# Performance work log

Measured on AMD Instinct MI355X. Metric: run time of the kernel, lower is better.

Reference implementation:

```python
import jax, jax.numpy as jnp
import numpy as np

H = 512


def setup_inputs() -> dict:
    key = jax.random.key(0)
    ks = jax.random.split(key, 20)
    B, S, T, V, WD = 128, 80, 28, 8000, 1024
    sc = 0.02
    return {
        "encoder_hidden_state": jax.random.normal(ks[0], (1, B, H), jnp.float32),
        "encoder_outputs": jax.random.normal(ks[1], (B, S, H), jnp.float32),
        "target_sentences": jax.random.randint(ks[2], (B, T), 0, V),
        "training_steps": -200,
        "emb": jax.random.normal(ks[3], (V, WD), jnp.float32) * sc,
        "fc1_w": jax.random.normal(ks[4], (H, 2 * H), jnp.float32) * sc,
        "fc1_b": jnp.zeros((H,), jnp.float32),
        "fc2_w": jax.random.normal(ks[5], (H, H), jnp.float32) * sc,
        "fc2_b": jnp.zeros((H,), jnp.float32),
        "fc3_w": jax.random.normal(ks[6], (H, H), jnp.float32) * sc,
        "fc3_b": jnp.zeros((H,), jnp.float32),
        "fc4_w": jax.random.normal(ks[7], (H, H), jnp.float32) * sc,
        "fc4_b": jnp.zeros((H,), jnp.float32),
        "attn_w": jax.random.normal(ks[8], (H,), jnp.float32) * sc,
        "w_ih": jax.random.normal(ks[9], (4 * H, H + WD), jnp.float32) * sc,
        "w_hh": jax.random.normal(ks[10], (4 * H, H), jnp.float32) * sc,
        "b_ih": jnp.zeros((4 * H,), jnp.float32),
        "b_hh": jnp.zeros((4 * H,), jnp.float32),
        "out_w": jax.random.normal(ks[11], (V, H), jnp.float32) * sc,
        "out_b": jnp.zeros((V,), jnp.float32),
    }


def reference(encoder_hidden_state, encoder_outputs, target_sentences, training_steps,
              emb, fc1_w, fc1_b, fc2_w, fc2_b, fc3_w, fc3_b, fc4_w, fc4_b,
              attn_w, w_ih, w_hh, b_ih, b_hh, out_w, out_b):
    # With training_steps=-200, teacher-forcing threshold expit(-9.15)~1e-4, so
    # random.uniform(0.05,0.995) > threshold always holds -> target embedding used every step.
    tgt_emb = emb[target_sentences]              # (B, T, WD)
    xs = jnp.swapaxes(tgt_emb[:, :-1], 0, 1)     # (T-1, B, WD)
    h0 = encoder_hidden_state[0]                 # (B, H)
    c0 = jnp.zeros_like(h0)

    def step(carry, x_t):
        h, c = carry
        # additive-style attention: 4 stacked Linear layers (no nonlinearity, as in source)
        hs = jnp.broadcast_to(h[:, None, :], encoder_outputs.shape)
        z = jnp.concatenate([encoder_outputs, hs], axis=-1)      # (B, S, 2H)
        a = z @ fc1_w.T + fc1_b
        a = a @ fc2_w.T + fc2_b
        a = a @ fc3_w.T + fc3_b
        a = a @ fc4_w.T + fc4_b
        scores = a @ attn_w                                       # (B, S)
        wts = jax.nn.softmax(scores, axis=1)
        ctx = jnp.einsum('bs,bsd->bd', wts, encoder_outputs)      # (B, H)
        # single LSTM step (torch gate order i, f, g, o)
        li = jnp.concatenate([x_t, ctx], axis=1)                  # (B, WD+H)
        gates = li @ w_ih.T + b_ih + h @ w_hh.T + b_hh
        i_, f_, g_, o_ = jnp.split(gates, 4, axis=1)
        c_new = jax.nn.sigmoid(f_) * c + jax.nn.sigmoid(i_) * jnp.tanh(g_)
        h_new = jax.nn.sigmoid(o_) * jnp.tanh(c_new)
        logits = h_new @ out_w.T + out_b                          # (B, V)
        return (h_new, c_new), logits

    _, logits = jax.lax.scan(step, (h0, c0), xs)                  # (T-1, B, V)
    logits = jnp.swapaxes(logits, 0, 1)                           # (B, T-1, V)
    preds = jnp.argmax(logits, axis=2)
    return logits, preds
```

## Files before the change

### kernel.cpp

```cpp
#include <hip/hip_runtime.h>
#include <math.h>

#define BB 128
#define SS 80
#define HH 512
#define TT 27
#define TFULL 28
#define VV 8000

typedef __attribute__((ext_vector_type(4))) float f32x4;
typedef __attribute__((ext_vector_type(8))) short bfrag;

#define OFF_VA   0
#define OFF_VB   512
#define OFF_U    1024
#define OFF_PART 1536
#define OFF_CTX  17920
#define OFF_GB   83456
#define OFF_XG   345600
#define OFF_BAR  7423488
#define FP32_WS_FLOATS 7489536
#define O_H3     0
#define O_WHI    3670016
#define O_WLO    4718592
#define O_R      5767168
#define O_A3X    O_R
#define O_B3X    (O_R + 10616832)
#define O_B3L    O_R

__device__ __forceinline__ unsigned short f2bf(float x) {
    unsigned int u = __float_as_uint(x);
    unsigned int r = (u + 0x7fff + ((u >> 16) & 1)) >> 16;
    return (unsigned short)r;
}
__device__ __forceinline__ float bf2f(unsigned short h) {
    return __uint_as_float(((unsigned int)h) << 16);
}
__device__ __forceinline__ void gload16(void* lds, const void* g) {
    __builtin_amdgcn_global_load_lds(
        (__attribute__((address_space(1))) void*)g,
        (__attribute__((address_space(3))) void*)lds, 16, 0, 0);
}
__device__ __forceinline__ void gload16s(void* lds, const void* g) {
    __builtin_amdgcn_global_load_lds(
        (__attribute__((address_space(1))) void*)g,
        (__attribute__((address_space(3))) void*)lds, 16, 0, 1);
}

__global__ __launch_bounds__(256) void zero_bar(unsigned* b) {
    int i = blockIdx.x * 256 + threadIdx.x;
    if (i < 16512) b[i] = 0u;
}

__global__ __launch_bounds__(256) void conv_split(
    const float* __restrict__ src, int ld, int koff, int K,
    int mode, int bside, const int* __restrict__ gidx,
    unsigned short* __restrict__ dst)
{
    int r = blockIdx.x;
    int sr = r;
    if (mode == 1) { int b = r & 127, t = r >> 7; sr = gidx[b * TFULL + t]; }
    const float* s = src + (size_t)sr * ld + koff;
    unsigned short* d = dst + (size_t)r * (3 * K);
    int off_mid = bside ? 2 * K : K;
    int off_lo  = bside ? K : 2 * K;
    for (int c = threadIdx.x * 4; c < K; c += 1024) {
        float4 v = *(const float4*)(s + c);
        ushort4 hi, lo;
        hi.x = f2bf(v.x); lo.x = f2bf(v.x - bf2f(hi.x));
        hi.y = f2bf(v.y); lo.y = f2bf(v.y - bf2f(hi.y));
        hi.z = f2bf(v.z); lo.z = f2bf(v.z - bf2f(hi.z));
        hi.w = f2bf(v.w); lo.w = f2bf(v.w - bf2f(hi.w));
        *(ushort4*)(d + c) = hi;
        *(ushort4*)(d + off_mid + c) = hi;
        *(ushort4*)(d + off_lo + c) = lo;
    }
}

__global__ __launch_bounds__(256) void conv_splitc(
    const float* __restrict__ src, unsigned short* __restrict__ dst)
{
    int r = blockIdx.x;
    const float* s = src + (size_t)r * 512;
    unsigned short* d = dst + (size_t)r * 1024;
    int c = threadIdx.x * 2;
    float2 v = *(const float2*)(s + c);
    unsigned short hx = f2bf(v.x), hy = f2bf(v.y);
    d[c] = hx; d[c + 1] = hy;
    d[512 + c] = f2bf(v.x - bf2f(hx));
    d[512 + c + 1] = f2bf(v.y - bf2f(hy));
}

__global__ __launch_bounds__(256) void conv_splitw(
    const float* __restrict__ src,
    unsigned short* __restrict__ whi, unsigned short* __restrict__ wlo)
{
    int r = blockIdx.x;
    int sr = (r & 3) * 512 + (r >> 2);
    const float* s = src + (size_t)sr * 512;
    int c = threadIdx.x * 2;
    float2 v = *(const float2*)(s + c);
    unsigned short hx = f2bf(v.x), hy = f2bf(v.y);
    whi[(size_t)r * 512 + c] = hx;
    whi[(size_t)r * 512 + c + 1] = hy;
    wlo[(size_t)r * 512 + c] = f2bf(v.x - bf2f(hx));
    wlo[(size_t)r * 512 + c + 1] = f2bf(v.y - bf2f(hy));
}

__global__ __launch_bounds__(256) void gemm_bf16_nt(
    int M, int N, int K3,
    const unsigned short* __restrict__ A3, int astride, int ahalf,
    const unsigned short* __restrict__ B3,
    const float* __restrict__ bias,
    const float* __restrict__ addmat,
    float* __restrict__ C, int outMode)
{
    __shared__ unsigned short Asm[2][128 * 64];
    __shared__ unsigned short Bsm[2][128 * 64];
    int tid = threadIdx.x, wave = tid >> 6, lane = tid & 63;

    int nT = gridDim.x, mT = gridDim.y;
    int p = blockIdx.y * nT + blockIdx.x;
    int nwg = nT * mT;
    int q = nwg >> 3, rr = nwg & 7;
    int xcd = p & 7, pos = p >> 3;
    int lid = (xcd < rr) ? (xcd * (q + 1) + pos) : (rr * (q + 1) + (xcd - rr) * q + pos);
    const int GROUP = 9;
    int width = GROUP * nT;
    int gid2 = lid / width;
    int first_m = gid2 * GROUP;
    int gsz = mT - first_m; if (gsz > GROUP) gsz = GROUP;
    int rem = lid - gid2 * width;
    int mt = first_m + rem % gsz;
    int nt = rem / gsz;
    int m0 = mt * 128, n0 = nt * 128;

    int wm0 = (wave >> 1) * 64, wn0 = (wave & 1) * 64;
    f32x4 acc[4][4];
    #pragma unroll
    for (int i = 0; i < 4; ++i)
        #pragma unroll
        for (int j = 0; j < 4; ++j) acc[i][j] = (f32x4){0.f, 0.f, 0.f, 0.f};

    int srow8 = lane >> 3;
    int schunk = lane & 7;

    auto STAGE = [&](int buf, int k0) {
        int ek0 = ahalf ? (k0 >= 512 ? k0 - 512 : k0) : k0;
        #pragma unroll
        for (int rep = 0; rep < 4; ++rep) {
            int ci = wave * 4 + rep;
            int row = ci * 8 + srow8;
            int sc = schunk ^ (row & 7);
            int gm = m0 + row; if (gm >= M) gm = M - 1;
            gload16(Asm[buf] + ci * 512 + lane * 8,
                    A3 + (size_t)gm * astride + ek0 + sc * 8);
            int gn = n0 + row; if (gn >= N) gn = N - 1;
            gload16(Bsm[buf] + ci * 512 + lane * 8,
                    B3 + (size_t)gn * K3 + k0 + sc * 8);
        }
    };

    int nK = K3 >> 6;
    STAGE(0, 0);
    STAGE(1, 64);
    for (int kc = 0; kc < nK; ++kc) {
        if (kc < nK - 1) asm volatile("s_waitcnt vmcnt(8)" ::: "memory");
        else             asm volatile("s_waitcnt vmcnt(0)" ::: "memory");
        __builtin_amdgcn_s_barrier();
        const unsigned short* Ab = Asm[kc & 1];
        const unsigned short* Bb = Bsm[kc & 1];
        #pragma unroll
        for (int ks = 0; ks < 2; ++ks) {
            bfrag a[4], b[4];
            #pragma unroll
            for (int i = 0; i < 4; ++i) {
                int ar = wm0 + i * 16 + (lane & 15);
                int ab = (ar * 128 + ks * 64 + (lane >> 4) * 16) ^ ((ar & 7) << 4);
                a[i] = *(const bfrag*)((const char*)Ab + ab);
                int br = wn0 + i * 16 + (lane & 15);
                int bb = (br * 128 + ks * 64 + (lane >> 4) * 16) ^ ((br & 7) << 4);
                b[i] = *(const bfrag*)((const char*)Bb + bb);
            }
            #pragma unroll
            for (int i = 0; i < 4; ++i)
                #pragma unroll
                for (int j = 0; j < 4; ++j)
                    acc[i][j] = __builtin_amdgcn_mfma_f32_16x16x32_bf16(a[i], b[j], acc[i][j], 0, 0, 0);
        }
        __builtin_amdgcn_s_barrier();
        if (kc + 2 < nK) STAGE(kc & 1, (kc + 2) * 64);
    }
    #pragma unroll
    for (int i = 0; i < 4; ++i) {
        #pragma unroll
        for (int r = 0; r < 4; ++r) {
            int m = m0 + wm0 + i * 16 + ((lane >> 4) << 2) + r;
            if (m >= M) continue;
            #pragma unroll
            for (int j = 0; j < 4; ++j) {
                int n = n0 + wn0 + j * 16 + (lane & 15);
                if (n >= N) continue;
                float v = acc[i][j][r];
                if (bias) v += bias[n];
                if (addmat) v += addmat[(size_t)(m & 127) * 2048 + n];
                size_t oi;
                if (outMode == 0) oi = (size_t)m * N + n;
                else { int bb2 = m & 127, tt = m >> 7; oi = ((size_t)bb2 * TT + tt) * (size_t)VV + n; }
                __builtin_nontemporal_store(v, &C[oi]);
            }
        }
    }
}

__global__ __launch_bounds__(256, 1) void lstm_persist4(
    unsigned short* __restrict__ H3,
    const unsigned short* __restrict__ Whi,
    const unsigned short* __restrict__ Wlo,
    const float* __restrict__ xgb,
    unsigned* bar)
{
    __shared__ unsigned short Wl[64 * 512];
    __shared__ unsigned short Al[16 * 1024];
    __shared__ int s_ids[2];

    int tid = threadIdx.x, wv = tid >> 6, lane = tid & 63;
    if (tid == 0) {
        unsigned x;
        asm volatile("s_getreg_b32 %0, hwreg(HW_REG_XCC_ID)" : "=s"(x));
        x &= 7u;
        unsigned s = __hip_atomic_fetch_add(bar + 16384 + x * 16, 1u,
                        __ATOMIC_RELAXED, __HIP_MEMORY_SCOPE_AGENT);
        s_ids[0] = (int)x;
        s_ids[1] = (int)(s & 31u);
    }
    __syncthreads();
    int xcd = s_ids[0], slot = s_ids[1];
    int b0 = xcd * 16;
    int nq0 = slot * 64;

    int l15 = lane & 15, g4 = (lane >> 4) << 4;
    int arow = l15;
    int wr = wv * 16 + l15;
    int n_local = wv * 16 + l15;
    int g = n_local & 3;
    int kglob = slot * 16 + (n_local >> 2);
    const unsigned short* wloRow = Wlo + (size_t)(nq0 + n_local) * 512;
    float creg[4] = {0.f, 0.f, 0.f, 0.f};

    {
        const unsigned short* Wsrc = Whi + (size_t)nq0 * 512;
        #pragma unroll
        for (int j = 0; j < 16; ++j) {
            int ci = j * 256 + tid;
            int row = ci >> 6, cc = ci & 63;
            int sc = cc ^ (row & 7);
            gload16(Wl + ci * 8, Wsrc + (size_t)row * 512 + sc * 8);
        }
        asm volatile("s_waitcnt vmcnt(0)" ::: "memory");
    }
    __syncthreads();

    for (int t = 0; t < TT; ++t) {
        const unsigned short* Asrc = H3 + ((size_t)t * 128 + b0) * 1024;
        #pragma unroll
        for (int j = 0; j < 8; ++j) {
            int ci = j * 256 + tid;
            int row = ci >> 7, cc = ci & 127;
            int sc = cc ^ (row & 7);
            gload16s(Al + ci * 8, Asrc + (size_t)row * 1024 + sc * 8);
        }
        float xpre[4];
        #pragma unroll
        for (int r = 0; r < 4; ++r) {
            int m_local = ((lane >> 4) << 2) + r;
            xpre[r] = xgb[(((size_t)t * 128 + b0 + m_local) << 11) + (size_t)g * 512 + kglob];
        }
        asm volatile("s_waitcnt vmcnt(4)" ::: "memory");
        __builtin_amdgcn_s_barrier();

        f32x4 acc0 = (f32x4){0.f, 0.f, 0.f, 0.f};
        f32x4 acc1 = acc0;
        #pragma unroll
        for (int c = 0; c < 16; ++c) {
            int ab = (arow * 2048 + c * 64 + g4) ^ ((arow & 7) << 4);
            int wb = (wr * 1024 + c * 64 + g4) ^ ((wr & 7) << 4);
            bfrag a = *(const bfrag*)((const char*)Al + ab);
            bfrag w = *(const bfrag*)((const char*)Wl + wb);
            if (c & 1) acc1 = __builtin_amdgcn_mfma_f32_16x16x32_bf16(a, w, acc1, 0, 0, 0);
            else       acc0 = __builtin_amdgcn_mfma_f32_16x16x32_bf16(a, w, acc0, 0, 0, 0);
        }
        #pragma unroll
        for (int c = 0; c < 16; ++c) {
            int ab = (arow * 2048 + c * 64 + g4) ^ ((arow & 7) << 4);
            bfrag a = *(const bfrag*)((const char*)Al + ab);
            bfrag w = *(const bfrag*)(wloRow + c * 32 + (lane >> 4) * 8);
            if (c & 1) acc1 = __builtin_amdgcn_mfma_f32_16x16x32_bf16(a, w, acc1, 0, 0, 0);
            else       acc0 = __builtin_amdgcn_mfma_f32_16x16x32_bf16(a, w, acc0, 0, 0, 0);
        }
        #pragma unroll
        for (int c = 0; c < 16; ++c) {
            int ab = (arow * 2048 + (16 + c) * 64 + g4) ^ ((arow & 7) << 4);
            int wb = (wr * 1024 + c * 64 + g4) ^ ((wr & 7) << 4);
            bfrag a = *(const bfrag*)((const char*)Al + ab);
            bfrag w = *(const bfrag*)((const char*)Wl + wb);
            if (c & 1) acc1 = __builtin_amdgcn_mfma_f32_16x16x32_bf16(a, w, acc1, 0, 0, 0);
            else       acc0 = __builtin_amdgcn_mfma_f32_16x16x32_bf16(a, w, acc0, 0, 0, 0);
        }
        f32x4 accT = acc0 + acc1;

        #pragma unroll
        for (int r = 0; r < 4; ++r) {
            int m_local = ((lane >> 4) << 2) + r;
            int b = b0 + m_local;
            float v = accT[r] + xpre[r];
            float f1 = __shfl_down(v, 1);
            float f2 = __shfl_down(v, 2);
            float f3 = __shfl_down(v, 3);
            if ((lane & 3) == 0) {
                float si = 1.f / (1.f + expf(-v));
                float sf = 1.f / (1.f + expf(-f1));
                float tg = tanhf(f2);
                float so = 1.f / (1.f + expf(-f3));
                float cn = sf * creg[r] + si * tg;
                float hn = so * tanhf(cn);
                creg[r] = cn;
                unsigned short hi = f2bf(hn);
                unsigned short lo = f2bf(hn - bf2f(hi));
                unsigned short* hr = H3 + ((size_t)(t + 1) * 128 + b) * 1024;
                hr[kglob] = hi; hr[512 + kglob] = lo;
            }
        }

        if (t != TT - 1) {
            asm volatile("s_waitcnt vmcnt(0)" ::: "memory");
            __syncthreads();
            unsigned ph = (unsigned)(t + 1);
            if (tid == 0)
                __hip_atomic_store(bar + xcd * 2048 + slot * 16, ph,
                                   __ATOMIC_RELAXED, __HIP_MEMORY_SCOPE_AGENT);
            if (tid < 32) {
                unsigned* fl = bar + xcd * 2048 + tid * 16;
                while (__hip_atomic_load(fl, __ATOMIC_RELAXED,
                                         __HIP_MEMORY_SCOPE_AGENT) < ph)
                    __builtin_amdgcn_s_sleep(1);
            }
            __syncthreads();
        }
    }
}

__global__ __launch_bounds__(512) void matvec_col_partial(
    const float* __restrict__ W, int ldw, int koff,
    const float* __restrict__ vin, float* __restrict__ part)
{
    int k = threadIdx.x;
    int o0 = blockIdx.x * 16;
    float acc = 0.f;
    #pragma unroll
    for (int o = 0; o < 16; ++o)
        acc += W[(size_t)(o0 + o) * ldw + koff + k] * vin[o0 + o];
    part[blockIdx.x * 512 + k] = acc;
}

__global__ __launch_bounds__(512) void matvec_combine(
    const float* __restrict__ part, float* __restrict__ vout)
{
    int k = threadIdx.x;
    float s = 0.f;
    #pragma unroll
    for (int c = 0; c < 32; ++c) s += part[c * 512 + k];
    vout[k] = s;
}

__global__ __launch_bounds__(256) void attn_ctx(
    const float* __restrict__ enc, const float* __restrict__ u,
    float* __restrict__ ctx)
{
    __shared__ float su[HH];
    __shared__ float sw[SS];
    __shared__ float ssum;
    int b = blockIdx.x, tid = threadIdx.x;
    su[tid] = u[tid];
    su[tid + 256] = u[tid + 256];
    __syncthreads();
    const float* eb = enc + (size_t)b * SS * HH;
    int wave = tid >> 6, lane = tid & 63;
    for (int s = wave; s < SS; s += 4) {
        const float* row = eb + s * HH;
        float acc = 0.f;
        for (int k = lane; k < HH; k += 64) acc += row[k] * su[k];
        #pragma unroll
        for (int off = 32; off; off >>= 1) acc += __shfl_down(acc, off);
        if (lane == 0) sw[s] = acc;
    }
    __syncthreads();
    if (tid == 0) {
        float mx = sw[0];
        for (int s = 1; s < SS; ++s) mx = fmaxf(mx, sw[s]);
        float sum = 0.f;
        for (int s = 0; s < SS; ++s) { float e = expf(sw[s] - mx); sw[s] = e; sum += e; }
        ssum = sum;
    }
    __syncthreads();
    float inv = 1.0f / ssum;
    for (int k = tid; k < HH; k += 256) {
        float acc = 0.f;
        #pragma unroll 4
        for (int s = 0; s < SS; ++s) acc += sw[s] * eb[s * HH + k];
        ctx[(size_t)b * HH + k] = acc * inv;
    }
}

__global__ __launch_bounds__(256) void gemm_nt(
    int M, int N, int K,
    const float* __restrict__ A, int lda,
    const float* __restrict__ Bm, int ldb, int kob,
    const float* __restrict__ bias1, const float* __restrict__ bias2,
    float* __restrict__ C)
{
    __shared__ float As[16][132];
    __shared__ float Bs[16][132];
    int tid = threadIdx.x;
    int m0 = blockIdx.y * 128, n0 = blockIdx.x * 128;
    int tn = tid & 15, tm = tid >> 4;
    float acc[8][8];
    #pragma unroll
    for (int i = 0; i < 8; ++i)
        #pragma unroll
        for (int j = 0; j < 8; ++j) acc[i][j] = 0.f;
    int lr = tid >> 2;
    int lk = (tid & 3) * 4;
    for (int k0 = 0; k0 < K; k0 += 16) {
        #pragma unroll
        for (int half = 0; half < 2; ++half) {
            int mr = lr + half * 64;
            int m = m0 + mr;
            float4 va = make_float4(0.f, 0.f, 0.f, 0.f);
            if (m < M) va = *(const float4*)(A + (size_t)m * lda + k0 + lk);
            As[lk + 0][mr] = va.x; As[lk + 1][mr] = va.y;
            As[lk + 2][mr] = va.z; As[lk + 3][mr] = va.w;
            int n = n0 + mr;
            float4 vb = make_float4(0.f, 0.f, 0.f, 0.f);
            if (n < N) vb = *(const float4*)(Bm + (size_t)n * ldb + kob + k0 + lk);
            Bs[lk + 0][mr] = vb.x; Bs[lk + 1][mr] = vb.y;
            Bs[lk + 2][mr] = vb.z; Bs[lk + 3][mr] = vb.w;
        }
        __syncthreads();
        #pragma unroll
        for (int kk = 0; kk < 16; ++kk) {
            float4 a0 = *(const float4*)&As[kk][tm * 8];
            float4 a1 = *(const float4*)&As[kk][tm * 8 + 4];
            float4 b0 = *(const float4*)&Bs[kk][tn * 8];
            float4 b1 = *(const float4*)&Bs[kk][tn * 8 + 4];
            float av[8] = {a0.x, a0.y, a0.z, a0.w, a1.x, a1.y, a1.z, a1.w};
            float bv[8] = {b0.x, b0.y, b0.z, b0.w, b1.x, b1.y, b1.z, b1.w};
            #pragma unroll
            for (int i = 0; i < 8; ++i)
                #pragma unroll
                for (int j = 0; j < 8; ++j)
                    acc[i][j] += av[i] * bv[j];
        }
        __syncthreads();
    }
    #pragma unroll
    for (int i = 0; i < 8; ++i) {
        int m = m0 + tm * 8 + i;
        if (m >= M) continue;
        #pragma unroll
        for (int j = 0; j < 8; ++j) {
            int n = n0 + tn * 8 + j;
            if (n >= N) continue;
            float v = acc[i][j];
            if (bias1) v += bias1[n];
            if (bias2) v += bias2[n];
            C[(size_t)m * N + n] = v;
        }
    }
}

__global__ __launch_bounds__(256) void argmax_k(
    const float* __restrict__ logits, float* __restrict__ preds)
{
    int r = blockIdx.x * 4 + (threadIdx.x >> 6);
    int lane = threadIdx.x & 63;
    const float* row = logits + (size_t)r * VV;
    float best = -INFINITY;
    int bi = 0;
    for (int v = lane; v < VV; v += 64) {
        float x = row[v];
        if (x > best) { best = x; bi = v; }
    }
    #pragma unroll
    for (int off = 32; off; off >>= 1) {
        float ob = __shfl_down(best, off);
        int oi = __shfl_down(bi, off);
        if (ob > best || (ob == best && oi < bi)) { best = ob; bi = oi; }
    }
    if (lane == 0) preds[r] = (float)bi;
}

extern "C" void kernel_launch(void* const* d_in, const int* in_sizes, int n_in,
                              void* d_out, int out_size, void* d_ws, size_t ws_size,
                              hipStream_t stream) {
    const float* ehs   = (const float*)d_in[0];
    const float* enc   = (const float*)d_in[1];
    const int*   tgt   = (const int*)d_in[2];
    const float* emb   = (const float*)d_in[4];
    const float* fc1w  = (const float*)d_in[5];
    const float* fc2w  = (const float*)d_in[7];
    const float* fc3w  = (const float*)d_in[9];
    const float* fc4w  = (const float*)d_in[11];
    const float* attnw = (const float*)d_in[13];
    const float* wih   = (const float*)d_in[14];
    const float* whh   = (const float*)d_in[15];
    const float* bih   = (const float*)d_in[16];
    const float* bhh   = (const float*)d_in[17];
    const float* outw  = (const float*)d_in[18];
    const float* outb  = (const float*)d_in[19];
    float* out = (float*)d_out;
    float* ws  = (float*)d_ws;

    float* vA   = ws + OFF_VA;
    float* vB   = ws + OFF_VB;
    float* u    = ws + OFF_U;
    float* part = ws + OFF_PART;
    float* ctx  = ws + OFF_CTX;
    float* gb   = ws + OFF_GB;
    float* xg   = ws + OFF_XG;
    unsigned* bar = (unsigned*)(ws + OFF_BAR);
    unsigned short* bfb = (unsigned short*)(ws + FP32_WS_FLOATS);
    unsigned short* H3   = bfb + O_H3;
    unsigned short* WHI  = bfb + O_WHI;
    unsigned short* WLO  = bfb + O_WLO;
    unsigned short* A3X  = bfb + O_A3X;
    unsigned short* B3X  = bfb + O_B3X;
    unsigned short* B3L  = bfb + O_B3L;

    matvec_col_partial<<<32, 512, 0, stream>>>(fc4w, 512, 0, attnw, part);
    matvec_combine<<<1, 512, 0, stream>>>(part, vA);
    matvec_col_partial<<<32, 512, 0, stream>>>(fc3w, 512, 0, vA, part);
    matvec_combine<<<1, 512, 0, stream>>>(part, vB);
    matvec_col_partial<<<32, 512, 0, stream>>>(fc2w, 512, 0, vB, part);
    matvec_combine<<<1, 512, 0, stream>>>(part, vA);
    matvec_col_partial<<<32, 512, 0, stream>>>(fc1w, 1024, 0, vA, part);
    matvec_combine<<<1, 512, 0, stream>>>(part, u);

    attn_ctx<<<128, 256, 0, stream>>>(enc, u, ctx);

    {
        dim3 g(16, 1);
        gemm_nt<<<g, 256, 0, stream>>>(128, 2048, 512, ctx, 512,
                                       wih, 1536, 1024, bih, bhh, gb);
    }

    conv_split<<<2048, 256, 0, stream>>>(wih, 1536, 0, 1024, 0, 1, nullptr, B3X);
    conv_split<<<3456, 256, 0, stream>>>(emb, 1024, 0, 1024, 1, 0, tgt, A3X);
    {
        dim3 g(16, 27);
        gemm_bf16_nt<<<g, 256, 0, stream>>>(3456, 2048, 3072, A3X, 3072, 0, B3X,
                                            nullptr, gb, xg, 0);
    }

    conv_split<<<8000, 256, 0, stream>>>(outw, 512, 0, 512, 0, 1, nullptr, B3L);
    conv_splitw<<<2048, 256, 0, stream>>>(whh, WHI, WLO);
    conv_splitc<<<128, 256, 0, stream>>>(ehs, H3);

    zero_bar<<<65, 256, 0, stream>>>(bar);
    lstm_persist4<<<256, 256, 0, stream>>>(H3, WHI, WLO, xg, bar);

    {
        dim3 g(63, 27);
        gemm_bf16_nt<<<g, 256, 0, stream>>>(3456, 8000, 1536,
                                            H3 + (size_t)128 * 1024, 1024, 1, B3L,
                                            outb, nullptr, out, 1);
    }

    argmax_k<<<864, 256, 0, stream>>>(out, out + (size_t)TT * 128 * VV);
}
```

Before: 623.3 us.

## Store compact hi/lo bf16 splits and preload Whh low-part into registers

The split-bf16 conversion now writes only hi and lo halves (2K wide) instead of a duplicated 3K layout. The GEMM computes wrapped k-offsets for both A and B so the hi term is re-read from the compact buffer. This cuts conversion write traffic and the footprint of the workspace buffers. The LSTM kernel also loads its Whh low-part fragments into registers once instead of every timestep, and uses four accumulators to expose more MFMA independence, at the cost of higher register pressure.

```diff
diff --git a/kernel.cpp b/kernel.cpp
--- a/kernel.cpp
+++ b/kernel.cpp
@@ -25,7 +25,7 @@
 #define O_WLO    4718592
 #define O_R      5767168
 #define O_A3X    O_R
-#define O_B3X    (O_R + 10616832)
+#define O_B3X    (O_R + 7077888)
 #define O_B3L    O_R
 
 __device__ __forceinline__ unsigned short f2bf(float x) {
@@ -52,18 +52,16 @@
     if (i < 16512) b[i] = 0u;
 }
 
-__global__ __launch_bounds__(256) void conv_split(
-    const float* __restrict__ src, int ld, int koff, int K,
-    int mode, int bside, const int* __restrict__ gidx,
+__global__ __launch_bounds__(256) void conv_cpk(
+    const float* __restrict__ src, int ld, int K,
+    int mode, const int* __restrict__ gidx,
     unsigned short* __restrict__ dst)
 {
     int r = blockIdx.x;
     int sr = r;
     if (mode == 1) { int b = r & 127, t = r >> 7; sr = gidx[b * TFULL + t]; }
-    const float* s = src + (size_t)sr * ld + koff;
-    unsigned short* d = dst + (size_t)r * (3 * K);
-    int off_mid = bside ? 2 * K : K;
-    int off_lo  = bside ? K : 2 * K;
+    const float* s = src + (size_t)sr * ld;
+    unsigned short* d = dst + (size_t)r * (2 * K);
     for (int c = threadIdx.x * 4; c < K; c += 1024) {
         float4 v = *(const float4*)(s + c);
         ushort4 hi, lo;
@@ -72,23 +70,8 @@
         hi.z = f2bf(v.z); lo.z = f2bf(v.z - bf2f(hi.z));
         hi.w = f2bf(v.w); lo.w = f2bf(v.w - bf2f(hi.w));
         *(ushort4*)(d + c) = hi;
-        *(ushort4*)(d + off_mid + c) = hi;
-        *(ushort4*)(d + off_lo + c) = lo;
-    }
-}
-
-__global__ __launch_bounds__(256) void conv_splitc(
-    const float* __restrict__ src, unsigned short* __restrict__ dst)
-{
-    int r = blockIdx.x;
-    const float* s = src + (size_t)r * 512;
-    unsigned short* d = dst + (size_t)r * 1024;
-    int c = threadIdx.x * 2;
-    float2 v = *(const float2*)(s + c);
-    unsigned short hx = f2bf(v.x), hy = f2bf(v.y);
-    d[c] = hx; d[c + 1] = hy;
-    d[512 + c] = f2bf(v.x - bf2f(hx));
-    d[512 + c + 1] = f2bf(v.y - bf2f(hy));
+        *(ushort4*)(d + K + c) = lo;
+    }
 }
 
 __global__ __launch_bounds__(256) void conv_splitw(
@@ -109,8 +92,8 @@
 
 __global__ __launch_bounds__(256) void gemm_bf16_nt(
     int M, int N, int K3,
-    const unsigned short* __restrict__ A3, int astride, int ahalf,
-    const unsigned short* __restrict__ B3,
+    const unsigned short* __restrict__ A3, int astride, int aK,
+    const unsigned short* __restrict__ B3, int bstride, int bK,
     const float* __restrict__ bias,
     const float* __restrict__ addmat,
     float* __restrict__ C, int outMode)
@@ -146,7 +129,8 @@
     int schunk = lane & 7;
 
     auto STAGE = [&](int buf, int k0) {
-        int ek0 = ahalf ? (k0 >= 512 ? k0 - 512 : k0) : k0;
+        int ek0a = (k0 >= aK) ? k0 - aK : k0;
+        int ek0b = (k0 >= 2 * bK) ? k0 - 2 * bK : k0;
         #pragma unroll
         for (int rep = 0; rep < 4; ++rep) {
             int ci = wave * 4 + rep;
@@ -154,10 +138,10 @@
             int sc = schunk ^ (row & 7);
             int gm = m0 + row; if (gm >= M) gm = M - 1;
             gload16(Asm[buf] + ci * 512 + lane * 8,
-                    A3 + (size_t)gm * astride + ek0 + sc * 8);
+                    A3 + (size_t)gm * astride + ek0a + sc * 8);
             int gn = n0 + row; if (gn >= N) gn = N - 1;
             gload16(Bsm[buf] + ci * 512 + lane * 8,
-                    B3 + (size_t)gn * K3 + k0 + sc * 8);
+                    B3 + (size_t)gn * bstride + ek0b + sc * 8);
         }
     };
 
@@ -259,6 +243,10 @@
         }
         asm volatile("s_waitcnt vmcnt(0)" ::: "memory");
     }
+    bfrag wlo[16];
+    #pragma unroll
+    for (int c = 0; c < 16; ++c)
+        wlo[c] = *(const bfrag*)(wloRow + c * 32 + (lane >> 4) * 8);
     __syncthreads();
 
     for (int t = 0; t < TT; ++t) {
@@ -280,23 +268,30 @@
         __builtin_amdgcn_s_barrier();
 
         f32x4 acc0 = (f32x4){0.f, 0.f, 0.f, 0.f};
-        f32x4 acc1 = acc0;
+        f32x4 acc1 = acc0, acc2 = acc0, acc3 = acc0;
         #pragma unroll
         for (int c = 0; c < 16; ++c) {
             int ab = (arow * 2048 + c * 64 + g4) ^ ((arow & 7) << 4);
             int wb = (wr * 1024 + c * 64 + g4) ^ ((wr & 7) << 4);
             bfrag a = *(const bfrag*)((const char*)Al + ab);
             bfrag w = *(const bfrag*)((const char*)Wl + wb);
-            if (c & 1) acc1 = __builtin_amdgcn_mfma_f32_16x16x32_bf16(a, w, acc1, 0, 0, 0);
-            else       acc0 = __builtin_amdgcn_mfma_f32_16x16x32_bf16(a, w, acc0, 0, 0, 0);
+            switch (c & 3) {
+                case 0: acc0 = __builtin_amdgcn_mfma_f32_16x16x32_bf16(a, w, acc0, 0, 0, 0); break;
+                case 1: acc1 = __builtin_amdgcn_mfma_f32_16x16x32_bf16(a, w, acc1, 0, 0, 0); break;
+                case 2: acc2 = __builtin_amdgcn_mfma_f32_16x16x32_bf16(a, w, acc2, 0, 0, 0); break;
+                default: acc3 = __builtin_amdgcn_mfma_f32_16x16x32_bf16(a, w, acc3, 0, 0, 0); break;
+            }
         }
         #pragma unroll
         for (int c = 0; c < 16; ++c) {
             int ab = (arow * 2048 + c * 64 + g4) ^ ((arow & 7) << 4);
             bfrag a = *(const bfrag*)((const char*)Al + ab);
-            bfrag w = *(const bfrag*)(wloRow + c * 32 + (lane >> 4) * 8);
-            if (c & 1) acc1 = __builtin_amdgcn_mfma_f32_16x16x32_bf16(a, w, acc1, 0, 0, 0);
-            else       acc0 = __builtin_amdgcn_mfma_f32_16x16x32_bf16(a, w, acc0, 0, 0, 0);
+            switch (c & 3) {
+                case 0: acc0 = __builtin_amdgcn_mfma_f32_16x16x32_bf16(a, wlo[c], acc0, 0, 0, 0); break;
+                case 1: acc1 = __builtin_amdgcn_mfma_f32_16x16x32_bf16(a, wlo[c], acc1, 0, 0, 0); break;
+                case 2: acc2 = __builtin_amdgcn_mfma_f32_16x16x32_bf16(a, wlo[c], acc2, 0, 0, 0); break;
+                default: acc3 = __builtin_amdgcn_mfma_f32_16x16x32_bf16(a, wlo[c], acc3, 0, 0, 0); break;
+            }
         }
         #pragma unroll
         for (int c = 0; c < 16; ++c) {
@@ -304,10 +299,14 @@
             int wb = (wr * 1024 + c * 64 + g4) ^ ((wr & 7) << 4);
             bfrag a = *(const bfrag*)((const char*)Al + ab);
             bfrag w = *(const bfrag*)((const char*)Wl + wb);
-            if (c & 1) acc1 = __builtin_amdgcn_mfma_f32_16x16x32_bf16(a, w, acc1, 0, 0, 0);
-            else       acc0 = __builtin_amdgcn_mfma_f32_16x16x32_bf16(a, w, acc0, 0, 0, 0);
-        }
-        f32x4 accT = acc0 + acc1;
+            switch (c & 3) {
+                case 0: acc0 = __builtin_amdgcn_mfma_f32_16x16x32_bf16(a, w, acc0, 0, 0, 0); break;
+                case 1: acc1 = __builtin_amdgcn_mfma_f32_16x16x32_bf16(a, w, acc1, 0, 0, 0); break;
+                case 2: acc2 = __builtin_amdgcn_mfma_f32_16x16x32_bf16(a, w, acc2, 0, 0, 0); break;
+                default: acc3 = __builtin_amdgcn_mfma_f32_16x16x32_bf16(a, w, acc3, 0, 0, 0); break;
+            }
+        }
+        f32x4 accT = (acc0 + acc1) + (acc2 + acc3);
 
         #pragma unroll
         for (int r = 0; r < 4; ++r) {
@@ -554,17 +553,19 @@
                                        wih, 1536, 1024, bih, bhh, gb);
     }
 
-    conv_split<<<2048, 256, 0, stream>>>(wih, 1536, 0, 1024, 0, 1, nullptr, B3X);
-    conv_split<<<3456, 256, 0, stream>>>(emb, 1024, 0, 1024, 1, 0, tgt, A3X);
+    conv_cpk<<<2048, 256, 0, stream>>>(wih, 1536, 1024, 0, nullptr, B3X);
+    conv_cpk<<<3456, 256, 0, stream>>>(emb, 1024, 1024, 1, tgt, A3X);
     {
         dim3 g(16, 27);
-        gemm_bf16_nt<<<g, 256, 0, stream>>>(3456, 2048, 3072, A3X, 3072, 0, B3X,
+        gemm_bf16_nt<<<g, 256, 0, stream>>>(3456, 2048, 3072,
+                                            A3X, 2048, 1024,
+                                            B3X, 2048, 1024,
                                             nullptr, gb, xg, 0);
     }
 
-    conv_split<<<8000, 256, 0, stream>>>(outw, 512, 0, 512, 0, 1, nullptr, B3L);
+    conv_cpk<<<8000, 256, 0, stream>>>(outw, 512, 512, 0, nullptr, B3L);
     conv_splitw<<<2048, 256, 0, stream>>>(whh, WHI, WLO);
-    conv_splitc<<<128, 256, 0, stream>>>(ehs, H3);
+    conv_cpk<<<128, 256, 0, stream>>>(ehs, 512, 512, 0, nullptr, H3);
 
     zero_bar<<<65, 256, 0, stream>>>(bar);
     lstm_persist4<<<256, 256, 0, stream>>>(H3, WHI, WLO, xg, bar);
@@ -572,7 +573,8 @@
     {
         dim3 g(63, 27);
         gemm_bf16_nt<<<g, 256, 0, stream>>>(3456, 8000, 1536,
-                                            H3 + (size_t)128 * 1024, 1024, 1, B3L,
+                                            H3 + (size_t)128 * 1024, 1024, 512,
+                                            B3L, 1024, 512,
                                             outb, nullptr, out, 1);
     }
 
```

Result: faster. 571.6 us (-8.3%).
